# Optimization experiments

Measured on AMD Instinct MI355X. Metric: run time of the kernel, lower is better.

The kernel has to match this reference:

```python
import jax, jax.numpy as jnp
import numpy as np
from jax import lax

ML = 3      # mL: intermediate channels of the generated smoother
K = 7       # kernelSize of the generated per-sample kernels
HID = 100   # MLP hidden width


def _conv2d(x, w, pad):
    # x: [N,C,H,W], w: [O,I,kh,kw], 'same'-style padding `pad`
    return lax.conv_general_dilated(
        x, w, window_strides=(1, 1), padding=[(pad, pad), (pad, pad)],
        dimension_numbers=('NCHW', 'OIHW', 'NCHW'))


def _batch_conv2d(inputs, kernels, pad=1):
    # grouped conv trick: inputs [B,1,H,W], kernels [B,1,kh,kw] -> [B,1,H,W]
    B, _, H, W = inputs.shape
    out = lax.conv_general_dilated(
        inputs.reshape(1, B, H, W), kernels, window_strides=(1, 1),
        padding=[(pad, pad), (pad, pad)], feature_group_count=B,
        dimension_numbers=('NCHW', 'OIHW', 'NCHW'))
    return out.reshape(B, 1, H, W)


def setup_inputs() -> dict:
    key = jax.random.key(0)
    ks = jax.random.split(key, 11)
    B, N = 32, 1024
    out_dim = ML * K * K
    inp = {
        'x': jax.random.normal(ks[0], (B, 1, N, N), jnp.float32),
        'f': jax.random.normal(ks[1], (B, 1, N, N), jnp.float32),
        'kernelA': jax.random.normal(ks[2], (B, 1, 3, 3), jnp.float32) * 0.5,
        # fc1: Linear(9,100) -> ReLU -> Linear(100, mL*K*K)   (stored [in,out])
        'fc1_w1': jax.random.normal(ks[3], (9, HID), jnp.float32) / np.sqrt(9.0),
        'fc1_b1': jnp.zeros((HID,), jnp.float32),
        'fc1_w2': jax.random.normal(ks[4], (HID, out_dim), jnp.float32) / np.sqrt(HID),
        'fc1_b2': jnp.zeros((out_dim,), jnp.float32),
        'fc2_w1': jax.random.normal(ks[5], (9, HID), jnp.float32) / np.sqrt(9.0),
        'fc2_b1': jnp.zeros((HID,), jnp.float32),
        'fc2_w2': jax.random.normal(ks[6], (HID, out_dim), jnp.float32) / np.sqrt(HID),
        'fc2_b2': jnp.zeros((out_dim,), jnp.float32),
    }
    return inp


def reference(x, f, kernelA, fc1_w1, fc1_b1, fc1_w2, fc1_b2,
              fc2_w1, fc2_b1, fc2_w2, fc2_b2):
    B = x.shape[0]
    pad = K // 2
    w = kernelA.reshape(B, 9)                                  # flatten(kernelA, 1)
    h1 = jax.nn.relu(w @ fc1_w1 + fc1_b1)
    weight1 = (h1 @ fc1_w2 + fc1_b2).reshape(B, ML, 1, K, K)
    h2 = jax.nn.relu(w @ fc2_w1 + fc2_b1)
    weight2 = (h2 @ fc2_w2 + fc2_b2).reshape(B, 1, ML, K, K)

    Ax = _batch_conv2d(x, kernelA, pad=1)
    r = f - Ax                                                 # residual [B,1,N,N]

    def per_sample(ri, w1, w2):
        # ri: [1,N,N]; w1: [mL,1,K,K]; w2: [1,mL,K,K]
        tmp = _conv2d(ri[None], w1, pad)                       # [1,mL,N,N]
        return _conv2d(tmp, w2, pad)[0]                        # [1,N,N]

    G2 = jax.vmap(per_sample)(r, weight1, weight2)             # [B,1,N,N]
    return x + G2
```

## Files before the change

kernel.cpp:

```cpp
#include <hip/hip_runtime.h>

#define N    1024
#define BSZ  32
#define PS   480
#define HID  100

__global__ __launch_bounds__(256) void prep_kernel(
    const float* __restrict__ kernelA,
    const float* __restrict__ fc1_w1, const float* __restrict__ fc1_b1,
    const float* __restrict__ fc1_w2, const float* __restrict__ fc1_b2,
    const float* __restrict__ fc2_w1, const float* __restrict__ fc2_b1,
    const float* __restrict__ fc2_w2, const float* __restrict__ fc2_b2,
    float* __restrict__ params)
{
    int b = blockIdx.x, t = threadIdx.x;
    __shared__ float w[9], h1[HID], h2[HID], w1[147], w2[147];
    if (t < 9) w[t] = kernelA[b * 9 + t];
    __syncthreads();
    if (t < HID) {
        float s1 = fc1_b1[t], s2 = fc2_b1[t];
        #pragma unroll
        for (int i = 0; i < 9; ++i) {
            s1 = fmaf(w[i], fc1_w1[i * HID + t], s1);
            s2 = fmaf(w[i], fc2_w1[i * HID + t], s2);
        }
        h1[t] = fmaxf(s1, 0.f);
        h2[t] = fmaxf(s2, 0.f);
    }
    __syncthreads();
    if (t < 147) {
        float s1 = fc1_b2[t], s2 = fc2_b2[t];
        for (int i = 0; i < HID; ++i) {
            s1 = fmaf(h1[i], fc1_w2[i * 147 + t], s1);
            s2 = fmaf(h2[i], fc2_w2[i * 147 + t], s2);
        }
        w1[t] = s1;
        w2[t] = s2;
    }
    __syncthreads();
    float* P = params + b * PS;
    if (t < 169) {
        int ey = t / 13, ex = t % 13;
        float s = 0.f;
        for (int m = 0; m < 3; ++m)
            for (int d1y = 0; d1y < 7; ++d1y) {
                int d2y = ey - d1y;
                if (d2y < 0 || d2y > 6) continue;
                for (int d1x = 0; d1x < 7; ++d1x) {
                    int d2x = ex - d1x;
                    if (d2x < 0 || d2x > 6) continue;
                    s = fmaf(w1[m * 49 + d1y * 7 + d1x],
                             w2[m * 49 + d2y * 7 + d2x], s);
                }
            }
        P[t] = s;
    }
    if (t < 147) { P[169 + t] = w1[t]; P[316 + t] = w2[t]; }
    if (t < 9)   P[463 + t] = w[t];
}

#define TR  64
#define TC  128
#define RRW 76
#define RC  140
#define QPR 35
#define NQ  (RRW * QPR)

__device__ __forceinline__ void conv_row4(const float* win, const float* __restrict__ P,
                                          int ky, float* accRow)
{
    #pragma unroll
    for (int c = 0; c < 13; ++c) {
        float tv = P[ky * 13 + c];
        #pragma unroll
        for (int j = 0; j < 4; ++j)
            accRow[j] = fmaf(win[c + j], tv, accRow[j]);
    }
}

__global__ __launch_bounds__(256, 3) void main_kernel(
    const float* __restrict__ X, const float* __restrict__ F,
    const float* __restrict__ params, float* __restrict__ out)
{
    __shared__ __align__(16) float rbuf[RRW * RC];
    const int t  = threadIdx.x;
    const int b  = blockIdx.z;
    const int y0 = blockIdx.y * TR;
    const int x0 = blockIdx.x * TC;
    const float* P  = params + b * PS;
    const float* Xb = X + (size_t)b * N * N;
    const float* Fb = F + (size_t)b * N * N;
    float*       Ob = out + (size_t)b * N * N;

    float ka[9];
    #pragma unroll
    for (int i = 0; i < 9; ++i) ka[i] = P[463 + i];

    for (int idx = t; idx < NQ; idx += 256) {
        int i  = idx / QPR;
        int j  = (idx - i * QPR) * 4;
        int gr = y0 - 6 + i;
        int gc = x0 - 6 + j;
        float4 v = make_float4(0.f, 0.f, 0.f, 0.f);
        if (gr >= 0 && gr < N) {
            float w8[3][8];
            #pragma unroll
            for (int dy = 0; dy < 3; ++dy) {
                int ry = gr - 1 + dy;
                float4 qa = make_float4(0.f, 0.f, 0.f, 0.f);
                float4 qb = make_float4(0.f, 0.f, 0.f, 0.f);
                if (ry >= 0 && ry < N) {
                    const float* xr = Xb + (size_t)ry * N;
                    if (gc - 2 >= 0 && gc + 1 < N)
                        qa = *reinterpret_cast<const float4*>(xr + gc - 2);
                    if (gc + 2 >= 0 && gc + 5 < N)
                        qb = *reinterpret_cast<const float4*>(xr + gc + 2);
                }
                w8[dy][0] = qa.x; w8[dy][1] = qa.y; w8[dy][2] = qa.z; w8[dy][3] = qa.w;
                w8[dy][4] = qb.x; w8[dy][5] = qb.y; w8[dy][6] = qb.z; w8[dy][7] = qb.w;
            }
            float s[4] = {0.f, 0.f, 0.f, 0.f};
            #pragma unroll
            for (int dy = 0; dy < 3; ++dy)
                #pragma unroll
                for (int dx = 0; dx < 3; ++dx) {
                    float kv = ka[dy * 3 + dx];
                    #pragma unroll
                    for (int c = 0; c < 4; ++c)
                        s[c] = fmaf(kv, w8[dy][c + dx + 1], s[c]);
                }
            const float* fr = Fb + (size_t)gr * N;
            if (gc >= 0 && gc + 1 < N) {
                float2 f0 = *reinterpret_cast<const float2*>(fr + gc);
                v.x = f0.x - s[0]; v.y = f0.y - s[1];
            }
            if (gc + 2 >= 0 && gc + 3 < N) {
                float2 f1 = *reinterpret_cast<const float2*>(fr + gc + 2);
                v.z = f1.x - s[2]; v.w = f1.y - s[3];
            }
        }
        *reinterpret_cast<float4*>(&rbuf[i * RC + j]) = v;
    }
    __syncthreads();

    const int tx4 = (t & 31) * 4;
    const int ty8 = (t >> 5) * 8;
    const float* rb = &rbuf[ty8 * RC + tx4];

    float acc[8][4] = {{0.f,0.f,0.f,0.f},{0.f,0.f,0.f,0.f},
                       {0.f,0.f,0.f,0.f},{0.f,0.f,0.f,0.f},
                       {0.f,0.f,0.f,0.f},{0.f,0.f,0.f,0.f},
                       {0.f,0.f,0.f,0.f},{0.f,0.f,0.f,0.f}};
    float win[16];

    #define LOAD_WIN(rr)                                                      \
        { float4 v0 = *reinterpret_cast<const float4*>(rb + (rr) * RC);       \
          float4 v1 = *reinterpret_cast<const float4*>(rb + (rr) * RC + 4);   \
          float4 v2 = *reinterpret_cast<const float4*>(rb + (rr) * RC + 8);   \
          float4 v3 = *reinterpret_cast<const float4*>(rb + (rr) * RC + 12);  \
          win[0]=v0.x; win[1]=v0.y; win[2]=v0.z; win[3]=v0.w;                 \
          win[4]=v1.x; win[5]=v1.y; win[6]=v1.z; win[7]=v1.w;                 \
          win[8]=v2.x; win[9]=v2.y; win[10]=v2.z; win[11]=v2.w;               \
          win[12]=v3.x; win[13]=v3.y; win[14]=v3.z; win[15]=v3.w; }

    #pragma unroll
    for (int rr = 0; rr < 20; ++rr) {
        LOAD_WIN(rr);
        const int ilo = (rr - 12 > 0) ? rr - 12 : 0;
        const int ihi = (rr < 7) ? rr : 7;
        #pragma unroll
        for (int i = ilo; i <= ihi; ++i)
            conv_row4(win, P, rr - i, acc[i]);
    }

    #pragma unroll
    for (int i = 0; i < 8; ++i) {
        const int gy = y0 + ty8 + i;
        const float4 xq = *reinterpret_cast<const float4*>(
            &Xb[(size_t)gy * N + x0 + tx4]);
        float4 o;
        o.x = xq.x + acc[i][0]; o.y = xq.y + acc[i][1];
        o.z = xq.z + acc[i][2]; o.w = xq.w + acc[i][3];
        *reinterpret_cast<float4*>(&Ob[(size_t)gy * N + x0 + tx4]) = o;
    }
}

#define SEG 64
#define AXX 14
#define AXU (SEG + 14)
#define ARR 12
#define ARU (SEG + 12)
#define ATA 6
#define ATU (SEG + 6)

__global__ __launch_bounds__(256) void border_kernel(
    const float* __restrict__ X, const float* __restrict__ F,
    const float* __restrict__ params, float* __restrict__ out)
{
    __shared__ float xs[AXX * AXU];
    __shared__ float rs[ARR * ARU];
    __shared__ float tmp[3 * ATA * ATU];
    __shared__ float sw1[147], sw2[147];

    const int  t    = threadIdx.x;
    const int  b    = blockIdx.y;
    const int  seg  = blockIdx.x;
    const int  edge = seg >> 4;
    const int  s    = seg & 15;
    const bool vert = edge >= 2;
    const bool hi   = (edge == 1) || (edge == 3);
    const int  T0   = hi ? (N - 6) : 0;
    const int  V0   = hi ? (N - 3) : 0;
    const int  D    = hi ? 3 : 0;
    const int  u0   = vert ? (3 + s * SEG) : (s * SEG);
    const int  acr0x = T0 - 4, al0x = u0 - 7;
    const int  acr0r = T0 - 3, al0r = u0 - 6;

    const float* P  = params + b * PS;
    const float* Xb = X + (size_t)b * N * N;
    const float* Fb = F + (size_t)b * N * N;
    float*       Ob = out + (size_t)b * N * N;

    if (t < 147) { sw1[t] = P[169 + t]; sw2[t] = P[316 + t]; }
    float ka[9];
    #pragma unroll
    for (int i = 0; i < 9; ++i) ka[i] = P[463 + i];

    for (int idx = t; idx < AXX * AXU; idx += 256) {
        int a = vert ? (idx % AXX) : (idx / AXU);
        int u = vert ? (idx / AXX) : (idx % AXU);
        int ga = acr0x + a, gl = al0x + u;
        int gy = vert ? gl : ga, gx = vert ? ga : gl;
        xs[a * AXU + u] =
            (gy >= 0 && gy < N && gx >= 0 && gx < N) ? Xb[gy * N + gx] : 0.f;
    }
    __syncthreads();

    for (int idx = t; idx < ARR * ARU; idx += 256) {
        int a = vert ? (idx % ARR) : (idx / ARU);
        int u = vert ? (idx / ARR) : (idx % ARU);
        int ga = acr0r + a, gl = al0r + u;
        int gy = vert ? gl : ga, gx = vert ? ga : gl;
        float v = 0.f;
        if (gy >= 0 && gy < N && gx >= 0 && gx < N) {
            float sc = 0.f;
            #pragma unroll
            for (int da = 0; da < 3; ++da)
                #pragma unroll
                for (int dl = 0; dl < 3; ++dl)
                    sc = fmaf(ka[vert ? (dl * 3 + da) : (da * 3 + dl)],
                              xs[(a + da) * AXU + (u + dl)], sc);
            v = Fb[gy * N + gx] - sc;
        }
        rs[a * ARU + u] = v;
    }
    __syncthreads();

    for (int idx = t; idx < 3 * ATA * ATU; idx += 256) {
        int m   = idx / (ATA * ATU);
        int rem = idx - m * (ATA * ATU);
        int a = rem / ATU, u = rem % ATU;
        int gl = (u0 - 3) + u;
        float sc = 0.f;
        if (gl >= 0 && gl < N) {
            #pragma unroll
            for (int da = 0; da < 7; ++da)
                #pragma unroll
                for (int dl = 0; dl < 7; ++dl)
                    sc = fmaf(sw1[m * 49 + (vert ? (dl * 7 + da) : (da * 7 + dl))],
                              rs[(a + da) * ARU + (u + dl)], sc);
        }
        tmp[idx] = sc;
    }
    __syncthreads();

    for (int idx = t; idx < 3 * SEG; idx += 256) {
        int v = idx / SEG, u = idx - (idx / SEG) * SEG;
        int gl = u0 + u, ga = V0 + v;
        if (vert && gl >= N - 3) continue;
        float sc = 0.f;
        #pragma unroll
        for (int m = 0; m < 3; ++m)
            #pragma unroll
            for (int d2a = 0; d2a < 7; ++d2a) {
                int aT = v + d2a - 3 + D;
                if (aT < 0 || aT >= ATA) continue;
                #pragma unroll
                for (int d2l = 0; d2l < 7; ++d2l)
                    sc = fmaf(sw2[m * 49 + (vert ? (d2l * 7 + d2a) : (d2a * 7 + d2l))],
                              tmp[(m * ATA + aT) * ATU + (u + d2l)], sc);
            }
        int gy = vert ? gl : ga, gx = vert ? ga : gl;
        float xv = xs[(ga - acr0x) * AXU + (gl - al0x)];
        Ob[gy * N + gx] = xv + sc;
    }
}

extern "C" void kernel_launch(void* const* d_in, const int* in_sizes, int n_in,
                              void* d_out, int out_size, void* d_ws, size_t ws_size,
                              hipStream_t stream)
{
    const float* x    = (const float*)d_in[0];
    const float* f    = (const float*)d_in[1];
    const float* kA   = (const float*)d_in[2];
    const float* f1w1 = (const float*)d_in[3];
    const float* f1b1 = (const float*)d_in[4];
    const float* f1w2 = (const float*)d_in[5];
    const float* f1b2 = (const float*)d_in[6];
    const float* f2w1 = (const float*)d_in[7];
    const float* f2b1 = (const float*)d_in[8];
    const float* f2w2 = (const float*)d_in[9];
    const float* f2b2 = (const float*)d_in[10];
    float* out    = (float*)d_out;
    float* params = (float*)d_ws;

    prep_kernel<<<BSZ, 256, 0, stream>>>(kA, f1w1, f1b1, f1w2, f1b2,
                                         f2w1, f2b1, f2w2, f2b2, params);
    main_kernel<<<dim3(N / TC, N / TR, BSZ), 256, 0, stream>>>(x, f, params, out);
    border_kernel<<<dim3(64, BSZ), 256, 0, stream>>>(x, f, params, out);
}
```

Baseline: 598.9 us.

## Halve main-kernel tile height and hoist composed-kernel taps into registers in groups

Reduces the tile from 64 to 32 rows, so each thread computes 4 output rows instead of 8, and raises the launch-bounds occupancy target from 3 to 6 blocks. The 13x13 composed kernel taps are loaded into registers five rows at a time, and windows are double-buffered through a hand-scheduled fully unrolled sequence instead of being read from global params inside the loop. The aim is to cut repeated global/scalar parameter loads and raise occupancy. In exchange, the 6-row halo becomes a larger share of each smaller tile, so there is more redundant residual recomputation and LDS traffic per output.

```diff
diff --git a/kernel.cpp b/kernel.cpp
--- a/kernel.cpp
+++ b/kernel.cpp
@@ -59,26 +59,45 @@
     if (t < 9)   P[463 + t] = w[t];
 }
 
-#define TR  64
+#define TR  32
 #define TC  128
-#define RRW 76
+#define RRW 44
 #define RC  140
 #define QPR 35
 #define NQ  (RRW * QPR)
 
-__device__ __forceinline__ void conv_row4(const float* win, const float* __restrict__ P,
-                                          int ky, float* accRow)
-{
-    #pragma unroll
-    for (int c = 0; c < 13; ++c) {
-        float tv = P[ky * 13 + c];
-        #pragma unroll
-        for (int j = 0; j < 4; ++j)
-            accRow[j] = fmaf(win[c + j], tv, accRow[j]);
-    }
-}
-
-__global__ __launch_bounds__(256, 3) void main_kernel(
+#define DECL_ROW(R, base)                                                     \
+    const float R##_0 = P[(base)],      R##_1 = P[(base) + 1],                \
+                R##_2 = P[(base) + 2],  R##_3 = P[(base) + 3],                \
+                R##_4 = P[(base) + 4],  R##_5 = P[(base) + 5],                \
+                R##_6 = P[(base) + 6],  R##_7 = P[(base) + 7],                \
+                R##_8 = P[(base) + 8],  R##_9 = P[(base) + 9],                \
+                R##_10 = P[(base) + 10], R##_11 = P[(base) + 11],             \
+                R##_12 = P[(base) + 12];
+
+#define CRC(w, R, a, c)                                                       \
+    (a)[0] = fmaf((w)[(c) + 0], R##_##c, (a)[0]);                             \
+    (a)[1] = fmaf((w)[(c) + 1], R##_##c, (a)[1]);                             \
+    (a)[2] = fmaf((w)[(c) + 2], R##_##c, (a)[2]);                             \
+    (a)[3] = fmaf((w)[(c) + 3], R##_##c, (a)[3]);
+
+#define CR4(w, R, a) do {                                                     \
+    CRC(w, R, a, 0)  CRC(w, R, a, 1)  CRC(w, R, a, 2)  CRC(w, R, a, 3)        \
+    CRC(w, R, a, 4)  CRC(w, R, a, 5)  CRC(w, R, a, 6)  CRC(w, R, a, 7)        \
+    CRC(w, R, a, 8)  CRC(w, R, a, 9)  CRC(w, R, a, 10) CRC(w, R, a, 11)       \
+    CRC(w, R, a, 12) } while (0)
+
+#define LW(wn, rr) {                                                          \
+    float4 v0 = *reinterpret_cast<const float4*>(rb + (rr) * RC);             \
+    float4 v1 = *reinterpret_cast<const float4*>(rb + (rr) * RC + 4);         \
+    float4 v2 = *reinterpret_cast<const float4*>(rb + (rr) * RC + 8);         \
+    float4 v3 = *reinterpret_cast<const float4*>(rb + (rr) * RC + 12);        \
+    wn[0] = v0.x; wn[1] = v0.y; wn[2]  = v0.z; wn[3]  = v0.w;                 \
+    wn[4] = v1.x; wn[5] = v1.y; wn[6]  = v1.z; wn[7]  = v1.w;                 \
+    wn[8] = v2.x; wn[9] = v2.y; wn[10] = v2.z; wn[11] = v2.w;                 \
+    wn[12] = v3.x; wn[13] = v3.y; wn[14] = v3.z; wn[15] = v3.w; }
+
+__global__ __launch_bounds__(256, 6) void main_kernel(
     const float* __restrict__ X, const float* __restrict__ F,
     const float* __restrict__ params, float* __restrict__ out)
 {
@@ -144,38 +163,73 @@
     __syncthreads();
 
     const int tx4 = (t & 31) * 4;
-    const int ty8 = (t >> 5) * 8;
-    const float* rb = &rbuf[ty8 * RC + tx4];
-
-    float acc[8][4] = {{0.f,0.f,0.f,0.f},{0.f,0.f,0.f,0.f},
-                       {0.f,0.f,0.f,0.f},{0.f,0.f,0.f,0.f},
-                       {0.f,0.f,0.f,0.f},{0.f,0.f,0.f,0.f},
+    const int ty4 = (t >> 5) * 4;
+    const float* rb = &rbuf[ty4 * RC + tx4];
+
+    float acc[4][4] = {{0.f,0.f,0.f,0.f},{0.f,0.f,0.f,0.f},
                        {0.f,0.f,0.f,0.f},{0.f,0.f,0.f,0.f}};
-    float win[16];
-
-    #define LOAD_WIN(rr)                                                      \
-        { float4 v0 = *reinterpret_cast<const float4*>(rb + (rr) * RC);       \
-          float4 v1 = *reinterpret_cast<const float4*>(rb + (rr) * RC + 4);   \
-          float4 v2 = *reinterpret_cast<const float4*>(rb + (rr) * RC + 8);   \
-          float4 v3 = *reinterpret_cast<const float4*>(rb + (rr) * RC + 12);  \
-          win[0]=v0.x; win[1]=v0.y; win[2]=v0.z; win[3]=v0.w;                 \
-          win[4]=v1.x; win[5]=v1.y; win[6]=v1.z; win[7]=v1.w;                 \
-          win[8]=v2.x; win[9]=v2.y; win[10]=v2.z; win[11]=v2.w;               \
-          win[12]=v3.x; win[13]=v3.y; win[14]=v3.z; win[15]=v3.w; }
+    float winA[16], winB[16];
+
+    {
+        DECL_ROW(K0, 0)  DECL_ROW(K1, 13) DECL_ROW(K2, 26)
+        DECL_ROW(K3, 39) DECL_ROW(K4, 52)
+        LW(winA, 0) LW(winB, 1)
+        CR4(winA, K0, acc[0]);
+        LW(winA, 2)
+        CR4(winB, K1, acc[0]); CR4(winB, K0, acc[1]);
+        LW(winB, 3)
+        CR4(winA, K2, acc[0]); CR4(winA, K1, acc[1]); CR4(winA, K0, acc[2]);
+        LW(winA, 4)
+        CR4(winB, K3, acc[0]); CR4(winB, K2, acc[1]); CR4(winB, K1, acc[2]);
+        CR4(winB, K0, acc[3]);
+        LW(winB, 5)
+        CR4(winA, K4, acc[0]); CR4(winA, K3, acc[1]); CR4(winA, K2, acc[2]);
+        CR4(winA, K1, acc[3]);
+        LW(winA, 6)
+        CR4(winB, K4, acc[1]); CR4(winB, K3, acc[2]); CR4(winB, K2, acc[3]);
+        LW(winB, 7)
+        CR4(winA, K4, acc[2]); CR4(winA, K3, acc[3]);
+        CR4(winB, K4, acc[3]);
+    }
+    {
+        DECL_ROW(K0, 65)  DECL_ROW(K1, 78) DECL_ROW(K2, 91)
+        DECL_ROW(K3, 104) DECL_ROW(K4, 117)
+        LW(winA, 5) LW(winB, 6)
+        CR4(winA, K0, acc[0]);
+        LW(winA, 7)
+        CR4(winB, K1, acc[0]); CR4(winB, K0, acc[1]);
+        LW(winB, 8)
+        CR4(winA, K2, acc[0]); CR4(winA, K1, acc[1]); CR4(winA, K0, acc[2]);
+        LW(winA, 9)
+        CR4(winB, K3, acc[0]); CR4(winB, K2, acc[1]); CR4(winB, K1, acc[2]);
+        CR4(winB, K0, acc[3]);
+        LW(winB, 10)
+        CR4(winA, K4, acc[0]); CR4(winA, K3, acc[1]); CR4(winA, K2, acc[2]);
+        CR4(winA, K1, acc[3]);
+        LW(winA, 11)
+        CR4(winB, K4, acc[1]); CR4(winB, K3, acc[2]); CR4(winB, K2, acc[3]);
+        LW(winB, 12)
+        CR4(winA, K4, acc[2]); CR4(winA, K3, acc[3]);
+        CR4(winB, K4, acc[3]);
+    }
+    {
+        DECL_ROW(K0, 130) DECL_ROW(K1, 143) DECL_ROW(K2, 156)
+        LW(winA, 10) LW(winB, 11)
+        CR4(winA, K0, acc[0]);
+        LW(winA, 12)
+        CR4(winB, K1, acc[0]); CR4(winB, K0, acc[1]);
+        LW(winB, 13)
+        CR4(winA, K2, acc[0]); CR4(winA, K1, acc[1]); CR4(winA, K0, acc[2]);
+        LW(winA, 14)
+        CR4(winB, K2, acc[1]); CR4(winB, K1, acc[2]); CR4(winB, K0, acc[3]);
+        LW(winB, 15)
+        CR4(winA, K2, acc[2]); CR4(winA, K1, acc[3]);
+        CR4(winB, K2, acc[3]);
+    }
 
     #pragma unroll
-    for (int rr = 0; rr < 20; ++rr) {
-        LOAD_WIN(rr);
-        const int ilo = (rr - 12 > 0) ? rr - 12 : 0;
-        const int ihi = (rr < 7) ? rr : 7;
-        #pragma unroll
-        for (int i = ilo; i <= ihi; ++i)
-            conv_row4(win, P, rr - i, acc[i]);
-    }
-
-    #pragma unroll
-    for (int i = 0; i < 8; ++i) {
-        const int gy = y0 + ty8 + i;
+    for (int i = 0; i < 4; ++i) {
+        const int gy = y0 + ty4 + i;
         const float4 xq = *reinterpret_cast<const float4*>(
             &Xb[(size_t)gy * N + x0 + tx4]);
         float4 o;
```

New measurement: 510.1 us. 14.8% less time.

## Store residual tile in fp16 LDS and retile main conv to 2x8 outputs

Applied to the files above, without the earlier changes.

The residual tile is now stored in shared memory as fp16 instead of fp32, halving LDS footprint. The tile height drops from 64 to 32 rows and each thread computes a 2x8 output block instead of 8x4. Filter taps are held in registers in groups of rows, with two alternating row windows. Occupancy hint rises to 8 blocks per CU. In exchange, the residual loses precision and the halo overhead per output grows with the shorter tile.

```diff
diff --git a/kernel.cpp b/kernel.cpp
--- a/kernel.cpp
+++ b/kernel.cpp
@@ -1,4 +1,5 @@
 #include <hip/hip_runtime.h>
+#include <hip/hip_fp16.h>
 
 #define N    1024
 #define BSZ  32
@@ -59,30 +60,58 @@
     if (t < 9)   P[463 + t] = w[t];
 }
 
-#define TR  64
+#define TR  32
 #define TC  128
-#define RRW 76
-#define RC  140
+#define RRW 44
+#define RC_H 152
 #define QPR 35
 #define NQ  (RRW * QPR)
 
-__device__ __forceinline__ void conv_row4(const float* win, const float* __restrict__ P,
-                                          int ky, float* accRow)
-{
-    #pragma unroll
-    for (int c = 0; c < 13; ++c) {
-        float tv = P[ky * 13 + c];
-        #pragma unroll
-        for (int j = 0; j < 4; ++j)
-            accRow[j] = fmaf(win[c + j], tv, accRow[j]);
-    }
-}
-
-__global__ __launch_bounds__(256, 3) void main_kernel(
+struct WinH { uint4 a, b; uint2 c; };
+
+__device__ __forceinline__ float hval(const unsigned int* u, int h) {
+    const __half2 p = *reinterpret_cast<const __half2*>(u + (h >> 1));
+    return (h & 1) ? __high2float(p) : __low2float(p);
+}
+
+#define DECL_ROW(R, base)                                                     \
+    const float R##_0 = P[(base)],      R##_1 = P[(base) + 1],                \
+                R##_2 = P[(base) + 2],  R##_3 = P[(base) + 3],                \
+                R##_4 = P[(base) + 4],  R##_5 = P[(base) + 5],                \
+                R##_6 = P[(base) + 6],  R##_7 = P[(base) + 7],                \
+                R##_8 = P[(base) + 8],  R##_9 = P[(base) + 9],                \
+                R##_10 = P[(base) + 10], R##_11 = P[(base) + 11],             \
+                R##_12 = P[(base) + 12];
+
+#define CR8C(u, R, a, c)                                                      \
+    (a)[0] = fmaf(hval(u, (c) + 0), R##_##c, (a)[0]);                         \
+    (a)[1] = fmaf(hval(u, (c) + 1), R##_##c, (a)[1]);                         \
+    (a)[2] = fmaf(hval(u, (c) + 2), R##_##c, (a)[2]);                         \
+    (a)[3] = fmaf(hval(u, (c) + 3), R##_##c, (a)[3]);                         \
+    (a)[4] = fmaf(hval(u, (c) + 4), R##_##c, (a)[4]);                         \
+    (a)[5] = fmaf(hval(u, (c) + 5), R##_##c, (a)[5]);                         \
+    (a)[6] = fmaf(hval(u, (c) + 6), R##_##c, (a)[6]);                         \
+    (a)[7] = fmaf(hval(u, (c) + 7), R##_##c, (a)[7]);
+
+#define CR8(w, R, a) do {                                                     \
+    const unsigned int* _u = reinterpret_cast<const unsigned int*>(&(w));     \
+    CR8C(_u, R, a, 0)  CR8C(_u, R, a, 1)  CR8C(_u, R, a, 2)                   \
+    CR8C(_u, R, a, 3)  CR8C(_u, R, a, 4)  CR8C(_u, R, a, 5)                   \
+    CR8C(_u, R, a, 6)  CR8C(_u, R, a, 7)  CR8C(_u, R, a, 8)                   \
+    CR8C(_u, R, a, 9)  CR8C(_u, R, a, 10) CR8C(_u, R, a, 11)                  \
+    CR8C(_u, R, a, 12) } while (0)
+
+#define LWH(w, rr) {                                                          \
+    const __half* _p = &rbuf_h[(trow + (rr)) * RC_H + tcol];                  \
+    (w).a = *reinterpret_cast<const uint4*>(_p);                              \
+    (w).b = *reinterpret_cast<const uint4*>(_p + 8);                          \
+    (w).c = *reinterpret_cast<const uint2*>(_p + 16); }
+
+__global__ __launch_bounds__(256, 8) void main_kernel(
     const float* __restrict__ X, const float* __restrict__ F,
     const float* __restrict__ params, float* __restrict__ out)
 {
-    __shared__ __align__(16) float rbuf[RRW * RC];
+    __shared__ __align__(16) __half rbuf_h[RRW * RC_H];
     const int t  = threadIdx.x;
     const int b  = blockIdx.z;
     const int y0 = blockIdx.y * TR;
@@ -139,49 +168,79 @@
                 v.z = f1.x - s[2]; v.w = f1.y - s[3];
             }
         }
-        *reinterpret_cast<float4*>(&rbuf[i * RC + j]) = v;
-    }
-    __syncthreads();
-
-    const int tx4 = (t & 31) * 4;
-    const int ty8 = (t >> 5) * 8;
-    const float* rb = &rbuf[ty8 * RC + tx4];
-
-    float acc[8][4] = {{0.f,0.f,0.f,0.f},{0.f,0.f,0.f,0.f},
-                       {0.f,0.f,0.f,0.f},{0.f,0.f,0.f,0.f},
-                       {0.f,0.f,0.f,0.f},{0.f,0.f,0.f,0.f},
-                       {0.f,0.f,0.f,0.f},{0.f,0.f,0.f,0.f}};
-    float win[16];
-
-    #define LOAD_WIN(rr)                                                      \
-        { float4 v0 = *reinterpret_cast<const float4*>(rb + (rr) * RC);       \
-          float4 v1 = *reinterpret_cast<const float4*>(rb + (rr) * RC + 4);   \
-          float4 v2 = *reinterpret_cast<const float4*>(rb + (rr) * RC + 8);   \
-          float4 v3 = *reinterpret_cast<const float4*>(rb + (rr) * RC + 12);  \
-          win[0]=v0.x; win[1]=v0.y; win[2]=v0.z; win[3]=v0.w;                 \
-          win[4]=v1.x; win[5]=v1.y; win[6]=v1.z; win[7]=v1.w;                 \
-          win[8]=v2.x; win[9]=v2.y; win[10]=v2.z; win[11]=v2.w;               \
-          win[12]=v3.x; win[13]=v3.y; win[14]=v3.z; win[15]=v3.w; }
+        __half2 p0, p1;
+        p0.x = __float2half_rn(v.x); p0.y = __float2half_rn(v.y);
+        p1.x = __float2half_rn(v.z); p1.y = __float2half_rn(v.w);
+        uint2 st;
+        st.x = *reinterpret_cast<unsigned int*>(&p0);
+        st.y = *reinterpret_cast<unsigned int*>(&p1);
+        *reinterpret_cast<uint2*>(&rbuf_h[i * RC_H + j]) = st;
+    }
+    __syncthreads();
+
+    const int tcol = (t & 15) * 8;
+    const int trow = (t >> 4) * 2;
+
+    float acc0[8] = {0.f,0.f,0.f,0.f,0.f,0.f,0.f,0.f};
+    float acc1[8] = {0.f,0.f,0.f,0.f,0.f,0.f,0.f,0.f};
+    WinH wA, wB;
+
+    {
+        DECL_ROW(K0, 0)  DECL_ROW(K1, 13) DECL_ROW(K2, 26)
+        DECL_ROW(K3, 39) DECL_ROW(K4, 52)
+        LWH(wA, 0) LWH(wB, 1)
+        CR8(wA, K0, acc0);
+        LWH(wA, 2)
+        CR8(wB, K1, acc0); CR8(wB, K0, acc1);
+        LWH(wB, 3)
+        CR8(wA, K2, acc0); CR8(wA, K1, acc1);
+        LWH(wA, 4)
+        CR8(wB, K3, acc0); CR8(wB, K2, acc1);
+        LWH(wB, 5)
+        CR8(wA, K4, acc0); CR8(wA, K3, acc1);
+        CR8(wB, K4, acc1);
+    }
+    {
+        DECL_ROW(K5, 65)  DECL_ROW(K6, 78) DECL_ROW(K7, 91)
+        DECL_ROW(K8, 104) DECL_ROW(K9, 117)
+        LWH(wA, 5) LWH(wB, 6)
+        CR8(wA, K5, acc0);
+        LWH(wA, 7)
+        CR8(wB, K6, acc0); CR8(wB, K5, acc1);
+        LWH(wB, 8)
+        CR8(wA, K7, acc0); CR8(wA, K6, acc1);
+        LWH(wA, 9)
+        CR8(wB, K8, acc0); CR8(wB, K7, acc1);
+        LWH(wB, 10)
+        CR8(wA, K9, acc0); CR8(wA, K8, acc1);
+        CR8(wB, K9, acc1);
+    }
+    {
+        DECL_ROW(K10, 130) DECL_ROW(K11, 143) DECL_ROW(K12, 156)
+        LWH(wA, 10) LWH(wB, 11)
+        CR8(wA, K10, acc0);
+        LWH(wA, 12)
+        CR8(wB, K11, acc0); CR8(wB, K10, acc1);
+        LWH(wB, 13)
+        CR8(wA, K12, acc0); CR8(wA, K11, acc1);
+        CR8(wB, K12, acc1);
+    }
 
     #pragma unroll
-    for (int rr = 0; rr < 20; ++rr) {
-        LOAD_WIN(rr);
-        const int ilo = (rr - 12 > 0) ? rr - 12 : 0;
-        const int ihi = (rr < 7) ? rr : 7;
-        #pragma unroll
-        for (int i = ilo; i <= ihi; ++i)
-            conv_row4(win, P, rr - i, acc[i]);
-    }
-
-    #pragma unroll
-    for (int i = 0; i < 8; ++i) {
-        const int gy = y0 + ty8 + i;
-        const float4 xq = *reinterpret_cast<const float4*>(
-            &Xb[(size_t)gy * N + x0 + tx4]);
-        float4 o;
-        o.x = xq.x + acc[i][0]; o.y = xq.y + acc[i][1];
-        o.z = xq.z + acc[i][2]; o.w = xq.w + acc[i][3];
-        *reinterpret_cast<float4*>(&Ob[(size_t)gy * N + x0 + tx4]) = o;
+    for (int i = 0; i < 2; ++i) {
+        const int gy = y0 + trow + i;
+        const float* ac = (i == 0) ? acc0 : acc1;
+        const float4 x0q = *reinterpret_cast<const float4*>(
+            &Xb[(size_t)gy * N + x0 + tcol]);
+        const float4 x1q = *reinterpret_cast<const float4*>(
+            &Xb[(size_t)gy * N + x0 + tcol + 4]);
+        float4 o0, o1;
+        o0.x = x0q.x + ac[0]; o0.y = x0q.y + ac[1];
+        o0.z = x0q.z + ac[2]; o0.w = x0q.w + ac[3];
+        o1.x = x1q.x + ac[4]; o1.y = x1q.y + ac[5];
+        o1.z = x1q.z + ac[6]; o1.w = x1q.w + ac[7];
+        *reinterpret_cast<float4*>(&Ob[(size_t)gy * N + x0 + tcol])     = o0;
+        *reinterpret_cast<float4*>(&Ob[(size_t)gy * N + x0 + tcol + 4]) = o1;
     }
 }
 
```

Measured after the change: 1.813 ms. +202.7%, slower.
